# Optimization experiments

Measured on AMD Instinct MI355X. Metric: run time of the kernel, lower is better.

Reference implementation:

```python
import jax, jax.numpy as jnp
import numpy as np

H = 1024          # hidden_size
A = 8             # num_actions
T = 64            # timesteps
N = 256           # batch (num envs)


def _gru_cell(x, h, Wih, Whh, bih, bhh):
    # torch.nn.GRUCell math; gate order (r, z, n)
    gi = x @ Wih.T + bih           # [N, 3H]
    gh = h @ Whh.T + bhh           # [N, 3H]
    i_r, i_z, i_n = jnp.split(gi, 3, axis=1)
    h_r, h_z, h_n = jnp.split(gh, 3, axis=1)
    r = jax.nn.sigmoid(i_r + h_r)
    z = jax.nn.sigmoid(i_z + h_z)
    n = jnp.tanh(i_n + r * h_n)
    return (1.0 - z) * n + z * h


def setup_inputs() -> dict:
    key = jax.random.key(0)
    ks = jax.random.split(key, 12)
    s = 0.02
    return {
        "c": jax.random.normal(ks[0], (T * N, H), jnp.float32),
        "hxs": jax.random.normal(ks[1], (N, 3 * H), jnp.float32),
        "masks": jnp.ones((T * N, 1), jnp.float32),
        "prev_action_one_hot": jnp.zeros((T * N, A), jnp.float32).at[jnp.arange(T * N), jax.random.randint(ks[2], (T * N,), 0, A)].set(1.0),
        "h_gru_Wih": s * jax.random.normal(ks[3], (3 * H, H), jnp.float32),
        "h_gru_Whh": s * jax.random.normal(ks[4], (3 * H, H), jnp.float32),
        "h_gru_bih": jnp.zeros((3 * H,), jnp.float32),
        "h_gru_bhh": jnp.zeros((3 * H,), jnp.float32),
        "f_gru_Wih": s * jax.random.normal(ks[5], (3 * H, H), jnp.float32),
        "f_gru_Whh": s * jax.random.normal(ks[6], (3 * H, H), jnp.float32),
        "f_gru_bih": jnp.zeros((3 * H,), jnp.float32),
        "f_gru_bhh": jnp.zeros((3 * H,), jnp.float32),
        "p_W": s * jax.random.normal(ks[7], (2 * H, 2 * H + A), jnp.float32),
        "p_b": jnp.zeros((2 * H,), jnp.float32),
        "q_W": s * jax.random.normal(ks[8], (2 * H, 2 * H + A), jnp.float32),
        "q_b": jnp.zeros((2 * H,), jnp.float32),
    }


def reference(c, hxs, masks, prev_action_one_hot,
              h_gru_Wih, h_gru_Whh, h_gru_bih, h_gru_bhh,
              f_gru_Wih, f_gru_Whh, f_gru_bih, f_gru_bhh,
              p_W, p_b, q_W, q_b):
    c3 = c.reshape(T, N, H)
    m3 = masks.reshape(T, N, 1)
    a3 = prev_action_one_hot.reshape(T, N, A)
    f0 = hxs[:, :H]
    h0 = hxs[:, H:2 * H]
    q0 = hxs[:, 2 * H:]

    def step(carry, xs):
        f, h, q_mu = carry
        c_t, m_t, a_t = xs
        p_in = jnp.concatenate([h, q_mu, a_t], axis=1) * m_t
        p_dist = p_in @ p_W.T + p_b                     # [N, 2H]
        p_mu = p_dist[:, :H]
        q_in = jnp.concatenate([f, c_t, a_t], axis=1) * m_t
        q_dist = q_in @ q_W.T + q_b                     # [N, 2H]
        q_mu_new = q_dist[:, :H]
        f_new = _gru_cell(c_t, f * m_t, f_gru_Wih, f_gru_Whh, f_gru_bih, f_gru_bhh)
        h_new = _gru_cell(p_mu, h * m_t, h_gru_Wih, h_gru_Whh, h_gru_bih, h_gru_bhh)
        return (f_new, h_new, q_mu_new), (p_dist, q_dist)

    (f, h, q_mu), (p_all, q_all) = jax.lax.scan(step, (f0, h0, q0), (c3, m3, a3))
    acc_p = p_all.reshape(T * N, 2 * H)
    acc_q = q_all.reshape(T * N, 2 * H)
    hxs_out = jnp.concatenate([f, h, q_mu], axis=1)
    return acc_p, acc_q, hxs_out
```

## Files before the change

kernel.cpp:

```cpp
#include <hip/hip_runtime.h>
#include <math.h>

typedef __attribute__((ext_vector_type(8))) __bf16 bf16x8;
typedef __attribute__((ext_vector_type(4))) float f32x4;

constexpr int H = 1024, T = 64, NB = 256, TWOH = 2048, THREEH = 3072;
constexpr long long OFF_Q  = 33554432LL;
constexpr long long OFF_HX = 67108864LL;
constexpr int LA = 6;

constexpr int R_PWH = 0, R_PWQ = 2048, R_QWF = 4096, R_QWC = 6144,
              R_FWIH = 8192, R_FWHH = 11264, R_HWIH = 14336, R_HWHH = 17408;

#define LD4(p) (*reinterpret_cast<const float4*>(p))

__device__ __forceinline__ float sigf(float x) { return 1.0f / (1.0f + expf(-x)); }

__device__ __forceinline__ void gload16(const void* g, void* l) {
    __builtin_amdgcn_global_load_lds(
        (const __attribute__((address_space(1))) uint32_t*)g,
        (__attribute__((address_space(3))) uint32_t*)l, 16, 0, 0);
}

__device__ __forceinline__ void st_bf_swz(__bf16* base, int n, int k, float v) {
    base[(size_t)n * 1024 + (((k >> 3) ^ (n & 7)) << 3) + (k & 7)] = (__bf16)v;
}

__device__ __forceinline__ void swz_rc(int i, int NR, int& rt, int& ct) {
    const int k = i & 7;
    const int m = i >> 3;
    ct = k + 8 * (m / NR);
    rt = m % NR;
}

#define FRAGOFF(rloc, gl) (((rloc) << 7) + ((((gl)) ^ ((rloc) & 7)) << 4))

template<int RT>
__device__ __forceinline__ void stage_tile(const char* g, char* l, int kb, int tid) {
    #pragma unroll
    for (int i = 0; i < RT / 32; ++i) {
        const int L = i * 4096 + tid * 16;
        gload16(g + (size_t)(L >> 7) * 2048 + (size_t)kb * 128 + (L & 127), l + L);
    }
}

__device__ __forceinline__ void mm128(
    int tid, char* sA, char* sB,
    const char* A, const char* B,
    f32x4 (&acc)[2][4])
{
    const int lane = tid & 63, w = tid >> 6;
    const int l15 = lane & 15, lg = lane >> 4;
    const int wr = w >> 1, wc = w & 1;
    int aoff[2][2], boff[4][2];
    #pragma unroll
    for (int fr = 0; fr < 2; ++fr)
        #pragma unroll
        for (int kk = 0; kk < 2; ++kk)
            aoff[fr][kk] = FRAGOFF(wr * 32 + fr * 16 + l15, kk * 4 + lg);
    #pragma unroll
    for (int fc = 0; fc < 4; ++fc)
        #pragma unroll
        for (int kk = 0; kk < 2; ++kk)
            boff[fc][kk] = FRAGOFF(wc * 64 + fc * 16 + l15, kk * 4 + lg);

    stage_tile<64>(A, sA, 0, tid);
    stage_tile<128>(B, sB, 0, tid);
    stage_tile<64>(A, sA + 8192, 1, tid);
    stage_tile<128>(B, sB + 16384, 1, tid);
    for (int kb = 0; kb < 16; ++kb) {
        const int kn = kb + 2;
        if (kn < 16) {
            const int bo = kn % 3;
            stage_tile<64>(A, sA + bo * 8192, kn, tid);
            stage_tile<128>(B, sB + bo * 16384, kn, tid);
            asm volatile("s_waitcnt vmcnt(12)" ::: "memory");
        } else if (kb + 1 < 16) {
            asm volatile("s_waitcnt vmcnt(6)" ::: "memory");
        } else {
            asm volatile("s_waitcnt vmcnt(0)" ::: "memory");
        }
        __builtin_amdgcn_s_barrier();
        __builtin_amdgcn_sched_barrier(0);
        const int bc = kb % 3;
        char* Ab = sA + bc * 8192;
        char* Bb = sB + bc * 16384;
        bf16x8 af[2][2], bv[4][2];
        #pragma unroll
        for (int fr = 0; fr < 2; ++fr)
            #pragma unroll
            for (int kk = 0; kk < 2; ++kk)
                af[fr][kk] = *reinterpret_cast<const bf16x8*>(Ab + aoff[fr][kk]);
        #pragma unroll
        for (int fc = 0; fc < 4; ++fc)
            #pragma unroll
            for (int kk = 0; kk < 2; ++kk)
                bv[fc][kk] = *reinterpret_cast<const bf16x8*>(Bb + boff[fc][kk]);
        __builtin_amdgcn_s_setprio(1);
        #pragma unroll
        for (int kk = 0; kk < 2; ++kk)
            #pragma unroll
            for (int fr = 0; fr < 2; ++fr)
                #pragma unroll
                for (int fc = 0; fc < 4; ++fc)
                    acc[fr][fc] = __builtin_amdgcn_mfma_f32_16x16x32_bf16(
                        af[fr][kk], bv[fc][kk], acc[fr][fc], 0, 0, 0);
        __builtin_amdgcn_s_setprio(0);
        __builtin_amdgcn_s_barrier();
        __builtin_amdgcn_sched_barrier(0);
    }
}

__device__ __forceinline__ void mm32g1(
    int tid, char* sA, char* sB,
    const char* A, const char* Bg,
    f32x4 (&aR)[2], f32x4 (&aZ)[2], f32x4 (&aN)[2])
{
    const int lane = tid & 63, w = tid >> 6;
    const int l15 = lane & 15, lg = lane >> 4;
    const int wr = w >> 1, wc = w & 1;
    int aoff[2], boff[2][2];
    #pragma unroll
    for (int kk = 0; kk < 2; ++kk)
        aoff[kk] = FRAGOFF(wr * 16 + l15, kk * 4 + lg);
    #pragma unroll
    for (int fc = 0; fc < 2; ++fc)
        #pragma unroll
        for (int kk = 0; kk < 2; ++kk)
            boff[fc][kk] = FRAGOFF(wc * 32 + fc * 16 + l15, kk * 4 + lg);

    auto stg = [&](int buf, int kb) {
        stage_tile<32>(A, sA + buf * 4096, kb, tid);
        #pragma unroll
        for (int g = 0; g < 3; ++g)
            stage_tile<64>(Bg + (size_t)g * 2097152, sB + buf * 24576 + g * 8192, kb, tid);
    };
    stg(0, 0);
    for (int kb = 0; kb < 16; ++kb) {
        if (kb + 1 < 16) {
            stg((kb + 1) & 1, kb + 1);
            asm volatile("s_waitcnt vmcnt(7)" ::: "memory");
        } else {
            asm volatile("s_waitcnt vmcnt(0)" ::: "memory");
        }
        __builtin_amdgcn_s_barrier();
        __builtin_amdgcn_sched_barrier(0);
        char* Ab = sA + (kb & 1) * 4096;
        char* Bb = sB + (kb & 1) * 24576;
        bf16x8 af[2];
        #pragma unroll
        for (int kk = 0; kk < 2; ++kk)
            af[kk] = *reinterpret_cast<const bf16x8*>(Ab + aoff[kk]);
        bf16x8 bvr[2][2], bvz[2][2], bvn[2][2];
        #pragma unroll
        for (int fc = 0; fc < 2; ++fc)
            #pragma unroll
            for (int kk = 0; kk < 2; ++kk) {
                bvr[fc][kk] = *reinterpret_cast<const bf16x8*>(Bb + boff[fc][kk]);
                bvz[fc][kk] = *reinterpret_cast<const bf16x8*>(Bb + 8192 + boff[fc][kk]);
                bvn[fc][kk] = *reinterpret_cast<const bf16x8*>(Bb + 16384 + boff[fc][kk]);
            }
        __builtin_amdgcn_s_setprio(1);
        #pragma unroll
        for (int kk = 0; kk < 2; ++kk)
            #pragma unroll
            for (int fc = 0; fc < 2; ++fc) {
                aR[fc] = __builtin_amdgcn_mfma_f32_16x16x32_bf16(af[kk], bvr[fc][kk], aR[fc], 0, 0, 0);
                aZ[fc] = __builtin_amdgcn_mfma_f32_16x16x32_bf16(af[kk], bvz[fc][kk], aZ[fc], 0, 0, 0);
                aN[fc] = __builtin_amdgcn_mfma_f32_16x16x32_bf16(af[kk], bvn[fc][kk], aN[fc], 0, 0, 0);
            }
        __builtin_amdgcn_s_setprio(0);
        __builtin_amdgcn_s_barrier();
        __builtin_amdgcn_sched_barrier(0);
    }
}

__device__ __forceinline__ void do_xq(int slice, int i, int tid, char* sA, char* sB,
    const char* cbfB, const char* Wb, const float* act, const float* qW, float* out)
{
    const int lane = tid & 63, w = tid >> 6;
    const int l15 = lane & 15, lg = lane >> 4;
    const int wr = w >> 1, wc = w & 1;
    int rt, ct; swz_rc(i, 4, rt, ct);
    const int row0 = rt * 64, col0 = ct * 128;
    const size_t grow0 = (size_t)slice * NB + row0;
    f32x4 acc[2][4] = {};
    mm128(tid, sA, sB, cbfB + grow0 * 2048, Wb + (size_t)(R_QWC + col0) * 2048, acc);
    #pragma unroll
    for (int fc = 0; fc < 4; ++fc) {
        const int gc = col0 + wc * 64 + fc * 16 + l15;
        const float* wp = qW + (size_t)gc * 2056 + 2048;
        float4 x0 = LD4(wp), x1 = LD4(wp + 4);
        #pragma unroll
        for (int fr = 0; fr < 2; ++fr)
            #pragma unroll
            for (int j = 0; j < 4; ++j) {
                const size_t n = grow0 + wr * 32 + fr * 16 + lg * 4 + j;
                const float* ar = act + n * 8;
                float4 a0 = LD4(ar), a1 = LD4(ar + 4);
                float dot = a0.x * x0.x + a0.y * x0.y + a0.z * x0.z + a0.w * x0.w
                          + a1.x * x1.x + a1.y * x1.y + a1.z * x1.z + a1.w * x1.w;
                out[OFF_Q + n * TWOH + gc] = acc[fr][fc][j] + dot;
            }
    }
}

__device__ __forceinline__ void do_gf(int slice, int i, int tid, char* sA, char* sB,
    const char* cbfB, const char* Wb, __bf16* Gfb)
{
    const int lane = tid & 63, w = tid >> 6;
    const int l15 = lane & 15, lg = lane >> 4;
    const int wr = w >> 1, wc = w & 1;
    int rt, ct; swz_rc(i, 4, rt, ct);
    const int row0 = rt * 64, col0 = ct * 128;
    f32x4 acc[2][4] = {};
    mm128(tid, sA, sB, cbfB + ((size_t)slice * NB + row0) * 2048,
          Wb + (size_t)(R_FWIH + col0) * 2048, acc);
    __bf16* gdst = Gfb + (size_t)(slice & 7) * NB * THREEH;
    #pragma unroll
    for (int fc = 0; fc < 4; ++fc) {
        const int gc = col0 + wc * 64 + fc * 16 + l15;
        #pragma unroll
        for (int fr = 0; fr < 2; ++fr)
            #pragma unroll
            for (int j = 0; j < 4; ++j) {
                const int n = row0 + wr * 32 + fr * 16 + lg * 4 + j;
                gdst[(size_t)n * THREEH + gc] = (__bf16)acc[fr][fc][j];
            }
    }
}

__device__ __forceinline__ void do_pq(int tt, int i, int tid, char* sA, char* sB,
    const __bf16* qmu_t, const char* Wb, const float* masks, const float* act,
    const float* pW, const float* pb, float* out)
{
    const int lane = tid & 63, w = tid >> 6;
    const int l15 = lane & 15, lg = lane >> 4;
    const int wr = w >> 1, wc = w & 1;
    int rt, ct; swz_rc(i, 4, rt, ct);
    const int row0 = rt * 64, col0 = ct * 128;
    f32x4 acc[2][4] = {};
    mm128(tid, sA, sB, (const char*)qmu_t + (size_t)row0 * 2048,
          Wb + (size_t)(R_PWQ + col0) * 2048, acc);
    const float* mrow = masks + (size_t)tt * NB;
    float* ob = out + (size_t)tt * NB * TWOH;
    #pragma unroll
    for (int fc = 0; fc < 4; ++fc) {
        const int gc = col0 + wc * 64 + fc * 16 + l15;
        const float* wp = pW + (size_t)gc * 2056 + 2048;
        float4 x0 = LD4(wp), x1 = LD4(wp + 4);
        const float bb = pb[gc];
        #pragma unroll
        for (int fr = 0; fr < 2; ++fr)
            #pragma unroll
            for (int j = 0; j < 4; ++j) {
                const int n = row0 + wr * 32 + fr * 16 + lg * 4 + j;
                const float* ar = act + ((size_t)tt * NB + n) * 8;
                float4 a0 = LD4(ar), a1 = LD4(ar + 4);
                float dot = a0.x * x0.x + a0.y * x0.y + a0.z * x0.z + a0.w * x0.w
                          + a1.x * x1.x + a1.y * x1.y + a1.z * x1.z + a1.w * x1.w;
                ob[(size_t)n * TWOH + gc] = acc[fr][fc][j] + mrow[n] * dot + bb;
            }
    }
}

__global__ __launch_bounds__(256) void wcvt_k(
    const float* __restrict__ pW, const float* __restrict__ qW,
    const float* __restrict__ fWih, const float* __restrict__ fWhh,
    const float* __restrict__ hWih, const float* __restrict__ hWhh,
    __bf16* __restrict__ Wbf)
{
    const long i = (long)blockIdx.x * 256 + threadIdx.x;
    const int row = (int)(i >> 7);
    const int G   = (int)i & 127;
    const float* src; int stride; int koff = 0; int r;
    if (row < 2048)       { src = pW;   stride = 2056; koff = 0;    r = row; }
    else if (row < 4096)  { src = pW;   stride = 2056; koff = 1024; r = row - 2048; }
    else if (row < 6144)  { src = qW;   stride = 2056; koff = 0;    r = row - 4096; }
    else if (row < 8192)  { src = qW;   stride = 2056; koff = 1024; r = row - 6144; }
    else if (row < 11264) { src = fWih; stride = 1024; r = row - 8192; }
    else if (row < 14336) { src = fWhh; stride = 1024; r = row - 11264; }
    else if (row < 17408) { src = hWih; stride = 1024; r = row - 14336; }
    else                  { src = hWhh; stride = 1024; r = row - 17408; }
    const float* p = src + (long)r * stride + koff + G * 8;
    float4 a = LD4(p), b = LD4(p + 4);
    bf16x8 v;
    v[0] = (__bf16)a.x; v[1] = (__bf16)a.y; v[2] = (__bf16)a.z; v[3] = (__bf16)a.w;
    v[4] = (__bf16)b.x; v[5] = (__bf16)b.y; v[6] = (__bf16)b.z; v[7] = (__bf16)b.w;
    *reinterpret_cast<bf16x8*>(Wbf + (size_t)row * 1024 + ((G ^ (row & 7)) << 3)) = v;
}

__global__ __launch_bounds__(256) void ccvt_k(const float* __restrict__ c,
                                              __bf16* __restrict__ cbf) {
    const long i = (long)blockIdx.x * 256 + threadIdx.x;
    const int row = (int)(i >> 7);
    const int G   = (int)i & 127;
    const float* p = c + (size_t)row * 1024 + G * 8;
    float4 a = LD4(p), b = LD4(p + 4);
    bf16x8 v;
    v[0] = (__bf16)a.x; v[1] = (__bf16)a.y; v[2] = (__bf16)a.z; v[3] = (__bf16)a.w;
    v[4] = (__bf16)b.x; v[5] = (__bf16)b.y; v[6] = (__bf16)b.z; v[7] = (__bf16)b.w;
    *reinterpret_cast<bf16x8*>(cbf + (size_t)row * 1024 + ((G ^ (row & 7)) << 3)) = v;
}

__global__ __launch_bounds__(256) void init2_k(
    const float* __restrict__ hxs, const float* __restrict__ masks,
    float* __restrict__ fst0, float* __restrict__ hst0,
    __bf16* __restrict__ fbm0, __bf16* __restrict__ hbm0, __bf16* __restrict__ qmub0)
{
    const int idx = blockIdx.x * 256 + threadIdx.x;
    const int arr = idx >> 15;
    const int g   = idx & 32767;
    const int n   = g >> 7;
    const int G   = g & 127;
    const float m0 = masks[n];
    const float* p = hxs + (size_t)n * THREEH + arr * 1024 + G * 8;
    float4 a = LD4(p), b = LD4(p + 4);
    __bf16* dstB = arr == 0 ? fbm0 : (arr == 1 ? hbm0 : qmub0);
    bf16x8 v;
    v[0] = (__bf16)(a.x * m0); v[1] = (__bf16)(a.y * m0);
    v[2] = (__bf16)(a.z * m0); v[3] = (__bf16)(a.w * m0);
    v[4] = (__bf16)(b.x * m0); v[5] = (__bf16)(b.y * m0);
    v[6] = (__bf16)(b.z * m0); v[7] = (__bf16)(b.w * m0);
    *reinterpret_cast<bf16x8*>(dstB + (size_t)n * 1024 + ((G ^ (n & 7)) << 3)) = v;
    if (arr < 2) {
        float* dstF = arr == 0 ? fst0 : hst0;
        *reinterpret_cast<float4*>(dstF + (size_t)n * 1024 + G * 8) = a;
        *reinterpret_cast<float4*>(dstF + (size_t)n * 1024 + G * 8 + 4) = b;
    }
}

__global__ __launch_bounds__(256) void pre_k(
    const char* __restrict__ cbfB, const char* __restrict__ Wb,
    const float* __restrict__ act, const float* __restrict__ qW,
    const __bf16* __restrict__ qmb0, const float* __restrict__ masks,
    const float* __restrict__ pW, const float* __restrict__ pb,
    __bf16* __restrict__ Gfb, float* __restrict__ out)
{
    __shared__ char smem[73728];
    if (blockIdx.x < LA * 160) {
        const int s = blockIdx.x / 160;
        const int i = blockIdx.x % 160;
        if (i < 64) do_xq(s, i, threadIdx.x, smem, smem + 24576, cbfB, Wb, act, qW, out);
        else        do_gf(s, i - 64, threadIdx.x, smem, smem + 24576, cbfB, Wb, Gfb);
    } else {
        do_pq(0, blockIdx.x - LA * 160, threadIdx.x, smem, smem + 24576,
              qmb0, Wb, masks, act, pW, pb, out);
    }
}

__global__ __launch_bounds__(256) void k1_k(
    int t,
    const __bf16* __restrict__ hbm, const __bf16* __restrict__ fbm,
    __bf16* __restrict__ qmubN,
    const float* __restrict__ masks, const float* __restrict__ act,
    const float* __restrict__ qb, const float* __restrict__ qW,
    const char* __restrict__ Wb,
    __bf16* __restrict__ pmub, float* __restrict__ Shh,
    const __bf16* __restrict__ Gfb,
    const float* __restrict__ fbih, const float* __restrict__ fbhh,
    const float* __restrict__ fstF, float* __restrict__ fstN, __bf16* __restrict__ fbmN,
    float* __restrict__ out)
{
    __shared__ char smem[73728];
    char* sA = smem;
    char* sB = smem + 24576;
    const int tid = threadIdx.x;
    const int lane = tid & 63, w = tid >> 6;
    const int l15 = lane & 15, lg = lane >> 4;
    const int wr = w >> 1, wc = w & 1;
    const float* mrow = masks + (size_t)t * NB;
    const float* mn   = masks + (size_t)(t + 1 < T ? t + 1 : t) * NB;
    int b = blockIdx.x;

    if (b < 64) {
        int rt, ct; swz_rc(b, 4, rt, ct);
        const int row0 = rt * 64, col0 = ct * 128;
        f32x4 acc[2][4] = {};
        mm128(tid, sA, sB, (const char*)hbm + (size_t)row0 * 2048,
              Wb + (size_t)(R_PWH + col0) * 2048, acc);
        float* ob = out + (size_t)t * NB * TWOH;
        #pragma unroll
        for (int fc = 0; fc < 4; ++fc) {
            const int gc = col0 + wc * 64 + fc * 16 + l15;
            #pragma unroll
            for (int fr = 0; fr < 2; ++fr)
                #pragma unroll
                for (int j = 0; j < 4; ++j) {
                    const int n = row0 + wr * 32 + fr * 16 + lg * 4 + j;
                    const float v = ob[(size_t)n * TWOH + gc] + acc[fr][fc][j];
                    ob[(size_t)n * TWOH + gc] = v;
                    if (gc < 1024) st_bf_swz(pmub, n, gc, v);
                }
        }
    } else if (b < 128) {
        int rt, ct; swz_rc(b - 64, 4, rt, ct);
        const int row0 = rt * 64, col0 = ct * 128;
        f32x4 acc[2][4] = {};
        mm128(tid, sA, sB, (const char*)fbm + (size_t)row0 * 2048,
              Wb + (size_t)(R_QWF + col0) * 2048, acc);
        float* ob = out + OFF_Q + (size_t)t * NB * TWOH;
        #pragma unroll
        for (int fc = 0; fc < 4; ++fc) {
            const int gc = col0 + wc * 64 + fc * 16 + l15;
            const float bb = qb[gc];
            #pragma unroll
            for (int fr = 0; fr < 2; ++fr)
                #pragma unroll
                for (int j = 0; j < 4; ++j) {
                    const int n = row0 + wr * 32 + fr * 16 + lg * 4 + j;
                    const float xq = ob[(size_t)n * TWOH + gc];
                    float v = acc[fr][fc][j] + mrow[n] * xq + bb;
                    ob[(size_t)n * TWOH + gc] = v;
                    if (gc < 1024) st_bf_swz(qmubN, n, gc, v * mn[n]);
                }
        }
    } else if (b < 224) {
        int rt, ct; swz_rc(b - 128, 4, rt, ct);
        const int row0 = rt * 64, col0 = ct * 128;
        f32x4 acc[2][4] = {};
        mm128(tid, sA, sB, (const char*)hbm + (size_t)row0 * 2048,
              Wb + (size_t)(R_HWHH + col0) * 2048, acc);
        #pragma unroll
        for (int fc = 0; fc < 4; ++fc) {
            const int gc = col0 + wc * 64 + fc * 16 + l15;
            #pragma unroll
            for (int fr = 0; fr < 2; ++fr)
                #pragma unroll
                for (int j = 0; j < 4; ++j) {
                    const int n = row0 + wr * 32 + fr * 16 + lg * 4 + j;
                    Shh[(size_t)n * THREEH + gc] = acc[fr][fc][j];
                }
        }
    } else {
        int rt, ct; swz_rc(b - 224, 8, rt, ct);
        const int row0 = rt * 32, col0 = ct * 64;
        f32x4 aR[2] = {}, aZ[2] = {}, aN[2] = {};
        mm32g1(tid, sA, sB, (const char*)fbm + (size_t)row0 * 2048,
               Wb + (size_t)(R_FWHH + col0) * 2048, aR, aZ, aN);
        const __bf16* gsl = Gfb + (size_t)(t & 7) * NB * THREEH;
        #pragma unroll
        for (int fc = 0; fc < 2; ++fc) {
            const int col = col0 + wc * 32 + fc * 16 + l15;
            const float br  = fbih[col] + fbhh[col];
            const float bz  = fbih[col + 1024] + fbhh[col + 1024];
            const float bni = fbih[col + 2048], bnh = fbhh[col + 2048];
            #pragma unroll
            for (int j = 0; j < 4; ++j) {
                const int n = row0 + wr * 16 + lg * 4 + j;
                const float gfr = (float)gsl[(size_t)n * THREEH + col];
                const float gfz = (float)gsl[(size_t)n * THREEH + col + 1024];
                const float gfn = (float)gsl[(size_t)n * THREEH + col + 2048];
                const float rg = sigf(gfr + aR[fc][j] + br);
                const float zg = sigf(gfz + aZ[fc][j] + bz);
                const float ng = tanhf(gfn + bni + rg * (aN[fc][j] + bnh));
                const float fm = fstF[(size_t)n * 1024 + col] * mrow[n];
                const float o = (1.f - zg) * ng + zg * fm;
                fstN[(size_t)n * 1024 + col] = o;
                st_bf_swz(fbmN, n, col, o * mn[n]);
            }
        }
    }
}

__global__ __launch_bounds__(256) void k2_k(
    int t,
    const __bf16* __restrict__ pmub, const __bf16* __restrict__ qmubN,
    const char* __restrict__ cbfB,
    const float* __restrict__ Shh,
    const float* __restrict__ hstF, float* __restrict__ hstN, __bf16* __restrict__ hbmN,
    const char* __restrict__ Wb,
    const float* __restrict__ hbih, const float* __restrict__ hbhh,
    const float* __restrict__ masks, const float* __restrict__ act,
    const float* __restrict__ pW, const float* __restrict__ pb,
    const float* __restrict__ qW,
    __bf16* __restrict__ Gfb, float* __restrict__ out)
{
    __shared__ char smem[73728];
    char* sA = smem;
    char* sB = smem + 24576;
    const int tid = threadIdx.x;
    const int lane = tid & 63, w = tid >> 6;
    const int l15 = lane & 15, lg = lane >> 4;
    const int wr = w >> 1, wc = w & 1;
    const float* mrow = masks + (size_t)t * NB;
    const float* mn   = masks + (size_t)(t + 1 < T ? t + 1 : t) * NB;
    const int b = blockIdx.x;

    if (b < 128) {
        int rt, ct; swz_rc(b, 8, rt, ct);
        const int row0 = rt * 32, col0 = ct * 64;
        f32x4 aR[2] = {}, aZ[2] = {}, aN[2] = {};
        mm32g1(tid, sA, sB, (const char*)pmub + (size_t)row0 * 2048,
               Wb + (size_t)(R_HWIH + col0) * 2048, aR, aZ, aN);
        #pragma unroll
        for (int fc = 0; fc < 2; ++fc) {
            const int col = col0 + wc * 32 + fc * 16 + l15;
            const float bri = hbih[col],        brh = hbhh[col];
            const float bzi = hbih[col + 1024], bzh = hbhh[col + 1024];
            const float bni = hbih[col + 2048], bnh = hbhh[col + 2048];
            #pragma unroll
            for (int j = 0; j < 4; ++j) {
                const int n = row0 + wr * 16 + lg * 4 + j;
                const float ghr = Shh[(size_t)n * THREEH + col];
                const float ghz = Shh[(size_t)n * THREEH + col + 1024];
                const float ghn = Shh[(size_t)n * THREEH + col + 2048];
                const float rg = sigf(aR[fc][j] + bri + ghr + brh);
                const float zg = sigf(aZ[fc][j] + bzi + ghz + bzh);
                const float ng = tanhf(aN[fc][j] + bni + rg * (ghn + bnh));
                const float hm = hstF[(size_t)n * 1024 + col] * mrow[n];
                const float o = (1.f - zg) * ng + zg * hm;
                hstN[(size_t)n * 1024 + col] = o;
                st_bf_swz(hbmN, n, col, o * mn[n]);
            }
        }
    } else if (b < 192) {
        if (t + 1 < T)
            do_pq(t + 1, b - 128, tid, sA, sB, qmubN, Wb, masks, act, pW, pb, out);
    } else if (b < 256) {
        if (t + LA < T)
            do_xq(t + LA, b - 192, tid, sA, sB, cbfB, Wb, act, qW, out);
    } else {
        if (t + LA < T)
            do_gf(t + LA, b - 256, tid, sA, sB, cbfB, Wb, Gfb);
    }
}

__global__ __launch_bounds__(256) void write_hxs_k(const float* __restrict__ fS,
                                                   const float* __restrict__ hS,
                                                   float* out) {
    const int i = blockIdx.x * 256 + threadIdx.x;
    const int n = i / THREEH;
    const int j = i - n * THREEH;
    float v;
    if (j < H)          v = fS[(size_t)n * H + j];
    else if (j < TWOH)  v = hS[(size_t)n * H + (j - H)];
    else                v = out[OFF_Q + ((size_t)(T - 1) * NB + n) * TWOH + (j - TWOH)];
    out[OFF_HX + i] = v;
}

extern "C" void kernel_launch(void* const* d_in, const int* in_sizes, int n_in,
                              void* d_out, int out_size, void* d_ws, size_t ws_size,
                              hipStream_t stream) {
    (void)in_sizes; (void)n_in; (void)out_size; (void)ws_size;

    const float* c     = (const float*)d_in[0];
    const float* hxs   = (const float*)d_in[1];
    const float* masks = (const float*)d_in[2];
    const float* act   = (const float*)d_in[3];
    const float* hWih  = (const float*)d_in[4];
    const float* hWhh  = (const float*)d_in[5];
    const float* hbih  = (const float*)d_in[6];
    const float* hbhh  = (const float*)d_in[7];
    const float* fWih  = (const float*)d_in[8];
    const float* fWhh  = (const float*)d_in[9];
    const float* fbih  = (const float*)d_in[10];
    const float* fbhh  = (const float*)d_in[11];
    const float* pW    = (const float*)d_in[12];
    const float* pb    = (const float*)d_in[13];
    const float* qW    = (const float*)d_in[14];
    const float* qb    = (const float*)d_in[15];

    float* out = (float*)d_out;
    char*  wsb = (char*)d_ws;

    __bf16* Wbf  = (__bf16*)(wsb);
    __bf16* cbf  = (__bf16*)(wsb + 41943040LL);
    float*  fst[2] = { (float*)(wsb + 75497472LL), (float*)(wsb + 76546048LL) };
    float*  hst[2] = { (float*)(wsb + 77594624LL), (float*)(wsb + 78643200LL) };
    __bf16* fbm[2] = { (__bf16*)(wsb + 79691776LL), (__bf16*)(wsb + 80216064LL) };
    __bf16* hbm[2] = { (__bf16*)(wsb + 80740352LL), (__bf16*)(wsb + 81264640LL) };
    __bf16* qmb[2] = { (__bf16*)(wsb + 81788928LL), (__bf16*)(wsb + 82313216LL) };
    __bf16* pmub   = (__bf16*)(wsb + 82837504LL);
    float*  Shh    = (float*)(wsb + 83361792LL);
    __bf16* Gfb    = (__bf16*)(wsb + 86507520LL);
    const char* Wb   = (const char*)Wbf;
    const char* cbfB = (const char*)cbf;

    wcvt_k <<<dim3(10240), dim3(256), 0, stream>>>(pW, qW, fWih, fWhh, hWih, hWhh, Wbf);
    ccvt_k <<<dim3(8192),  dim3(256), 0, stream>>>(c, cbf);
    init2_k<<<dim3(384),   dim3(256), 0, stream>>>(hxs, masks, fst[0], hst[0],
                                                   fbm[0], hbm[0], qmb[0]);
    pre_k  <<<dim3(LA * 160 + 64), dim3(256), 0, stream>>>(
        cbfB, Wb, act, qW, qmb[0], masks, pW, pb, Gfb, out);

    for (int t = 0; t < T; ++t) {
        const int cur = t & 1, nxt = cur ^ 1;
        k1_k<<<dim3(352), dim3(256), 0, stream>>>(
            t, hbm[cur], fbm[cur], qmb[nxt],
            masks, act, qb, qW, Wb, pmub, Shh, Gfb,
            fbih, fbhh, fst[cur], fst[nxt], fbm[nxt], out);
        k2_k<<<dim3(352), dim3(256), 0, stream>>>(
            t, pmub, qmb[nxt], cbfB, Shh,
            hst[cur], hst[nxt], hbm[nxt],
            Wb, hbih, hbhh, masks, act, pW, pb, qW, Gfb, out);
    }

    write_hxs_k<<<dim3(3072), dim3(256), 0, stream>>>(fst[0], hst[0], out);
}
```

Baseline: 2.144 ms.

## Hoist all xq GEMMs to pre-kernel, use 64-row fused-gate GRU tiles, rebalance k1/k2

The c-only q projection (xq) for all 64 timesteps now runs in one large pre-kernel instead of being interleaved per step. The GRU gate GEMMs switch from 32x64 tiles to 64-row tiles whose r/z/n weight rows are interleaved in the weight conversion, so one contiguous B tile feeds all three gates and the block count drops. The f-GRU update moves from k1 to k2, and gf lookahead work is split across both kernels, shrinking each per-step launch to 256 blocks. Tile-index swizzling is replaced with plain row-major mapping. This trades the L2-friendly swizzle and some parallelism for less per-step work and better reuse of operands.

After: 2.506 ms. 1.17x slower.

```diff
diff --git a/kernel.cpp b/kernel.cpp
--- a/kernel.cpp
+++ b/kernel.cpp
@@ -24,13 +24,6 @@
 
 __device__ __forceinline__ void st_bf_swz(__bf16* base, int n, int k, float v) {
     base[(size_t)n * 1024 + (((k >> 3) ^ (n & 7)) << 3) + (k & 7)] = (__bf16)v;
-}
-
-__device__ __forceinline__ void swz_rc(int i, int NR, int& rt, int& ct) {
-    const int k = i & 7;
-    const int m = i >> 3;
-    ct = k + 8 * (m / NR);
-    rt = m % NR;
 }
 
 #define FRAGOFF(rloc, gl) (((rloc) << 7) + ((((gl)) ^ ((rloc) & 7)) << 4))
@@ -111,64 +104,73 @@
     }
 }
 
-__device__ __forceinline__ void mm32g1(
+__device__ __forceinline__ void mm64g(
     int tid, char* sA, char* sB,
-    const char* A, const char* Bg,
-    f32x4 (&aR)[2], f32x4 (&aZ)[2], f32x4 (&aN)[2])
+    const char* A, const char* Bp,
+    f32x4 (&aR)[2][2], f32x4 (&aZ)[2][2], f32x4 (&aN)[2][2])
 {
     const int lane = tid & 63, w = tid >> 6;
     const int l15 = lane & 15, lg = lane >> 4;
     const int wr = w >> 1, wc = w & 1;
-    int aoff[2], boff[2][2];
-    #pragma unroll
-    for (int kk = 0; kk < 2; ++kk)
-        aoff[kk] = FRAGOFF(wr * 16 + l15, kk * 4 + lg);
-    #pragma unroll
-    for (int fc = 0; fc < 2; ++fc)
+    int aoff[2][2], boff[2][3][2];
+    #pragma unroll
+    for (int fr = 0; fr < 2; ++fr)
         #pragma unroll
         for (int kk = 0; kk < 2; ++kk)
-            boff[fc][kk] = FRAGOFF(wc * 32 + fc * 16 + l15, kk * 4 + lg);
-
+            aoff[fr][kk] = FRAGOFF(wr * 32 + fr * 16 + l15, kk * 4 + lg);
+    #pragma unroll
+    for (int cb = 0; cb < 2; ++cb)
+        #pragma unroll
+        for (int g = 0; g < 3; ++g)
+            #pragma unroll
+            for (int kk = 0; kk < 2; ++kk) {
+                const int v = wc * 96 + (cb * 3 + g) * 16 + l15;
+                boff[cb][g][kk] = FRAGOFF(v, kk * 4 + lg);
+            }
     auto stg = [&](int buf, int kb) {
-        stage_tile<32>(A, sA + buf * 4096, kb, tid);
-        #pragma unroll
-        for (int g = 0; g < 3; ++g)
-            stage_tile<64>(Bg + (size_t)g * 2097152, sB + buf * 24576 + g * 8192, kb, tid);
+        stage_tile<64>(A, sA + buf * 8192, kb, tid);
+        stage_tile<192>(Bp, sB + buf * 24576, kb, tid);
     };
     stg(0, 0);
     for (int kb = 0; kb < 16; ++kb) {
         if (kb + 1 < 16) {
             stg((kb + 1) & 1, kb + 1);
-            asm volatile("s_waitcnt vmcnt(7)" ::: "memory");
+            asm volatile("s_waitcnt vmcnt(8)" ::: "memory");
         } else {
             asm volatile("s_waitcnt vmcnt(0)" ::: "memory");
         }
         __builtin_amdgcn_s_barrier();
         __builtin_amdgcn_sched_barrier(0);
-        char* Ab = sA + (kb & 1) * 4096;
+        char* Ab = sA + (kb & 1) * 8192;
         char* Bb = sB + (kb & 1) * 24576;
-        bf16x8 af[2];
+        bf16x8 af[2][2];
+        #pragma unroll
+        for (int fr = 0; fr < 2; ++fr)
+            #pragma unroll
+            for (int kk = 0; kk < 2; ++kk)
+                af[fr][kk] = *reinterpret_cast<const bf16x8*>(Ab + aoff[fr][kk]);
+        bf16x8 bv[2][3][2];
+        #pragma unroll
+        for (int cb = 0; cb < 2; ++cb)
+            #pragma unroll
+            for (int g = 0; g < 3; ++g)
+                #pragma unroll
+                for (int kk = 0; kk < 2; ++kk)
+                    bv[cb][g][kk] = *reinterpret_cast<const bf16x8*>(Bb + boff[cb][g][kk]);
+        __builtin_amdgcn_s_setprio(1);
         #pragma unroll
         for (int kk = 0; kk < 2; ++kk)
-            af[kk] = *reinterpret_cast<const bf16x8*>(Ab + aoff[kk]);
-        bf16x8 bvr[2][2], bvz[2][2], bvn[2][2];
-        #pragma unroll
-        for (int fc = 0; fc < 2; ++fc)
-            #pragma unroll
-            for (int kk = 0; kk < 2; ++kk) {
-                bvr[fc][kk] = *reinterpret_cast<const bf16x8*>(Bb + boff[fc][kk]);
-                bvz[fc][kk] = *reinterpret_cast<const bf16x8*>(Bb + 8192 + boff[fc][kk]);
-                bvn[fc][kk] = *reinterpret_cast<const bf16x8*>(Bb + 16384 + boff[fc][kk]);
-            }
-        __builtin_amdgcn_s_setprio(1);
-        #pragma unroll
-        for (int kk = 0; kk < 2; ++kk)
-            #pragma unroll
-            for (int fc = 0; fc < 2; ++fc) {
-                aR[fc] = __builtin_amdgcn_mfma_f32_16x16x32_bf16(af[kk], bvr[fc][kk], aR[fc], 0, 0, 0);
-                aZ[fc] = __builtin_amdgcn_mfma_f32_16x16x32_bf16(af[kk], bvz[fc][kk], aZ[fc], 0, 0, 0);
-                aN[fc] = __builtin_amdgcn_mfma_f32_16x16x32_bf16(af[kk], bvn[fc][kk], aN[fc], 0, 0, 0);
-            }
+            #pragma unroll
+            for (int fr = 0; fr < 2; ++fr)
+                #pragma unroll
+                for (int cb = 0; cb < 2; ++cb) {
+                    aR[fr][cb] = __builtin_amdgcn_mfma_f32_16x16x32_bf16(
+                        af[fr][kk], bv[cb][0][kk], aR[fr][cb], 0, 0, 0);
+                    aZ[fr][cb] = __builtin_amdgcn_mfma_f32_16x16x32_bf16(
+                        af[fr][kk], bv[cb][1][kk], aZ[fr][cb], 0, 0, 0);
+                    aN[fr][cb] = __builtin_amdgcn_mfma_f32_16x16x32_bf16(
+                        af[fr][kk], bv[cb][2][kk], aN[fr][cb], 0, 0, 0);
+                }
         __builtin_amdgcn_s_setprio(0);
         __builtin_amdgcn_s_barrier();
         __builtin_amdgcn_sched_barrier(0);
@@ -181,8 +183,7 @@
     const int lane = tid & 63, w = tid >> 6;
     const int l15 = lane & 15, lg = lane >> 4;
     const int wr = w >> 1, wc = w & 1;
-    int rt, ct; swz_rc(i, 4, rt, ct);
-    const int row0 = rt * 64, col0 = ct * 128;
+    const int row0 = (i >> 4) * 64, col0 = (i & 15) * 128;
     const size_t grow0 = (size_t)slice * NB + row0;
     f32x4 acc[2][4] = {};
     mm128(tid, sA, sB, cbfB + grow0 * 2048, Wb + (size_t)(R_QWC + col0) * 2048, acc);
@@ -211,8 +212,7 @@
     const int lane = tid & 63, w = tid >> 6;
     const int l15 = lane & 15, lg = lane >> 4;
     const int wr = w >> 1, wc = w & 1;
-    int rt, ct; swz_rc(i, 4, rt, ct);
-    const int row0 = rt * 64, col0 = ct * 128;
+    const int row0 = (i / 24) * 64, col0 = (i % 24) * 128;
     f32x4 acc[2][4] = {};
     mm128(tid, sA, sB, cbfB + ((size_t)slice * NB + row0) * 2048,
           Wb + (size_t)(R_FWIH + col0) * 2048, acc);
@@ -237,8 +237,7 @@
     const int lane = tid & 63, w = tid >> 6;
     const int l15 = lane & 15, lg = lane >> 4;
     const int wr = w >> 1, wc = w & 1;
-    int rt, ct; swz_rc(i, 4, rt, ct);
-    const int row0 = rt * 64, col0 = ct * 128;
+    const int row0 = (i >> 4) * 64, col0 = (i & 15) * 128;
     f32x4 acc[2][4] = {};
     mm128(tid, sA, sB, (const char*)qmu_t + (size_t)row0 * 2048,
           Wb + (size_t)(R_PWQ + col0) * 2048, acc);
@@ -279,8 +278,20 @@
     else if (row < 6144)  { src = qW;   stride = 2056; koff = 0;    r = row - 4096; }
     else if (row < 8192)  { src = qW;   stride = 2056; koff = 1024; r = row - 6144; }
     else if (row < 11264) { src = fWih; stride = 1024; r = row - 8192; }
-    else if (row < 14336) { src = fWhh; stride = 1024; r = row - 11264; }
-    else if (row < 17408) { src = hWih; stride = 1024; r = row - 14336; }
+    else if (row < 14336) {
+        const int rp = row - 11264;
+        const int j = rp / 192, rem = rp % 192;
+        const int chunk = rem / 48, rem2 = rem % 48;
+        const int g = rem2 >> 4, cc = rem2 & 15;
+        src = fWhh; stride = 1024; r = g * 1024 + j * 64 + chunk * 16 + cc;
+    }
+    else if (row < 17408) {
+        const int rp = row - 14336;
+        const int j = rp / 192, rem = rp % 192;
+        const int chunk = rem / 48, rem2 = rem % 48;
+        const int g = rem2 >> 4, cc = rem2 & 15;
+        src = hWih; stride = 1024; r = g * 1024 + j * 64 + chunk * 16 + cc;
+    }
     else                  { src = hWhh; stride = 1024; r = row - 17408; }
     const float* p = src + (long)r * stride + koff + G * 8;
     float4 a = LD4(p), b = LD4(p + 4);
@@ -338,13 +349,14 @@
     __bf16* __restrict__ Gfb, float* __restrict__ out)
 {
     __shared__ char smem[73728];
-    if (blockIdx.x < LA * 160) {
-        const int s = blockIdx.x / 160;
-        const int i = blockIdx.x % 160;
-        if (i < 64) do_xq(s, i, threadIdx.x, smem, smem + 24576, cbfB, Wb, act, qW, out);
-        else        do_gf(s, i - 64, threadIdx.x, smem, smem + 24576, cbfB, Wb, Gfb);
+    const int b = blockIdx.x;
+    if (b < 4096) {
+        do_xq(b >> 6, b & 63, threadIdx.x, smem, smem + 24576, cbfB, Wb, act, qW, out);
+    } else if (b < 4096 + LA * 96) {
+        const int r = b - 4096;
+        do_gf(r / 96, r % 96, threadIdx.x, smem, smem + 24576, cbfB, Wb, Gfb);
     } else {
-        do_pq(0, blockIdx.x - LA * 160, threadIdx.x, smem, smem + 24576,
+        do_pq(0, b - 4096 - LA * 96, threadIdx.x, smem, smem + 24576,
               qmb0, Wb, masks, act, pW, pb, out);
     }
 }
@@ -352,14 +364,12 @@
 __global__ __launch_bounds__(256) void k1_k(
     int t,
     const __bf16* __restrict__ hbm, const __bf16* __restrict__ fbm,
-    __bf16* __restrict__ qmubN,
+    __bf16* __restrict__ qmubN, const char* __restrict__ cbfB,
     const float* __restrict__ masks, const float* __restrict__ act,
     const float* __restrict__ qb, const float* __restrict__ qW,
     const char* __restrict__ Wb,
     __bf16* __restrict__ pmub, float* __restrict__ Shh,
-    const __bf16* __restrict__ Gfb,
-    const float* __restrict__ fbih, const float* __restrict__ fbhh,
-    const float* __restrict__ fstF, float* __restrict__ fstN, __bf16* __restrict__ fbmN,
+    __bf16* __restrict__ Gfb,
     float* __restrict__ out)
 {
     __shared__ char smem[73728];
@@ -374,8 +384,7 @@
     int b = blockIdx.x;
 
     if (b < 64) {
-        int rt, ct; swz_rc(b, 4, rt, ct);
-        const int row0 = rt * 64, col0 = ct * 128;
+        const int row0 = (b >> 4) * 64, col0 = (b & 15) * 128;
         f32x4 acc[2][4] = {};
         mm128(tid, sA, sB, (const char*)hbm + (size_t)row0 * 2048,
               Wb + (size_t)(R_PWH + col0) * 2048, acc);
@@ -394,8 +403,8 @@
                 }
         }
     } else if (b < 128) {
-        int rt, ct; swz_rc(b - 64, 4, rt, ct);
-        const int row0 = rt * 64, col0 = ct * 128;
+        b -= 64;
+        const int row0 = (b >> 4) * 64, col0 = (b & 15) * 128;
         f32x4 acc[2][4] = {};
         mm128(tid, sA, sB, (const char*)fbm + (size_t)row0 * 2048,
               Wb + (size_t)(R_QWF + col0) * 2048, acc);
@@ -416,8 +425,8 @@
                 }
         }
     } else if (b < 224) {
-        int rt, ct; swz_rc(b - 128, 4, rt, ct);
-        const int row0 = rt * 64, col0 = ct * 128;
+        const int i = b - 128;
+        const int row0 = (i / 24) * 64, col0 = (i % 24) * 128;
         f32x4 acc[2][4] = {};
         mm128(tid, sA, sB, (const char*)hbm + (size_t)row0 * 2048,
               Wb + (size_t)(R_HWHH + col0) * 2048, acc);
@@ -433,44 +442,21 @@
                 }
         }
     } else {
-        int rt, ct; swz_rc(b - 224, 8, rt, ct);
-        const int row0 = rt * 32, col0 = ct * 64;
-        f32x4 aR[2] = {}, aZ[2] = {}, aN[2] = {};
-        mm32g1(tid, sA, sB, (const char*)fbm + (size_t)row0 * 2048,
-               Wb + (size_t)(R_FWHH + col0) * 2048, aR, aZ, aN);
-        const __bf16* gsl = Gfb + (size_t)(t & 7) * NB * THREEH;
-        #pragma unroll
-        for (int fc = 0; fc < 2; ++fc) {
-            const int col = col0 + wc * 32 + fc * 16 + l15;
-            const float br  = fbih[col] + fbhh[col];
-            const float bz  = fbih[col + 1024] + fbhh[col + 1024];
-            const float bni = fbih[col + 2048], bnh = fbhh[col + 2048];
-            #pragma unroll
-            for (int j = 0; j < 4; ++j) {
-                const int n = row0 + wr * 16 + lg * 4 + j;
-                const float gfr = (float)gsl[(size_t)n * THREEH + col];
-                const float gfz = (float)gsl[(size_t)n * THREEH + col + 1024];
-                const float gfn = (float)gsl[(size_t)n * THREEH + col + 2048];
-                const float rg = sigf(gfr + aR[fc][j] + br);
-                const float zg = sigf(gfz + aZ[fc][j] + bz);
-                const float ng = tanhf(gfn + bni + rg * (aN[fc][j] + bnh));
-                const float fm = fstF[(size_t)n * 1024 + col] * mrow[n];
-                const float o = (1.f - zg) * ng + zg * fm;
-                fstN[(size_t)n * 1024 + col] = o;
-                st_bf_swz(fbmN, n, col, o * mn[n]);
-            }
-        }
+        if (t + LA < T)
+            do_gf(t + LA, b - 224, tid, sA, sB, cbfB, Wb, Gfb);
     }
 }
 
 __global__ __launch_bounds__(256) void k2_k(
     int t,
     const __bf16* __restrict__ pmub, const __bf16* __restrict__ qmubN,
-    const char* __restrict__ cbfB,
+    const __bf16* __restrict__ fbm, const char* __restrict__ cbfB,
     const float* __restrict__ Shh,
     const float* __restrict__ hstF, float* __restrict__ hstN, __bf16* __restrict__ hbmN,
+    const float* __restrict__ fstF, float* __restrict__ fstN, __bf16* __restrict__ fbmN,
     const char* __restrict__ Wb,
     const float* __restrict__ hbih, const float* __restrict__ hbhh,
+    const float* __restrict__ fbih, const float* __restrict__ fbhh,
     const float* __restrict__ masks, const float* __restrict__ act,
     const float* __restrict__ pW, const float* __restrict__ pb,
     const float* __restrict__ qW,
@@ -487,42 +473,70 @@
     const float* mn   = masks + (size_t)(t + 1 < T ? t + 1 : t) * NB;
     const int b = blockIdx.x;
 
-    if (b < 128) {
-        int rt, ct; swz_rc(b, 8, rt, ct);
-        const int row0 = rt * 32, col0 = ct * 64;
-        f32x4 aR[2] = {}, aZ[2] = {}, aN[2] = {};
-        mm32g1(tid, sA, sB, (const char*)pmub + (size_t)row0 * 2048,
-               Wb + (size_t)(R_HWIH + col0) * 2048, aR, aZ, aN);
-        #pragma unroll
-        for (int fc = 0; fc < 2; ++fc) {
-            const int col = col0 + wc * 32 + fc * 16 + l15;
+    if (b < 64) {
+        const int row0 = (b >> 4) * 64, col0 = (b & 15) * 64;
+        f32x4 aR[2][2] = {}, aZ[2][2] = {}, aN[2][2] = {};
+        mm64g(tid, sA, sB, (const char*)pmub + (size_t)row0 * 2048,
+              Wb + (size_t)(R_HWIH + (b & 15) * 192) * 2048, aR, aZ, aN);
+        #pragma unroll
+        for (int cb = 0; cb < 2; ++cb) {
+            const int col = col0 + wc * 32 + cb * 16 + l15;
             const float bri = hbih[col],        brh = hbhh[col];
             const float bzi = hbih[col + 1024], bzh = hbhh[col + 1024];
             const float bni = hbih[col + 2048], bnh = hbhh[col + 2048];
             #pragma unroll
-            for (int j = 0; j < 4; ++j) {
-                const int n = row0 + wr * 16 + lg * 4 + j;
-                const float ghr = Shh[(size_t)n * THREEH + col];
-                const float ghz = Shh[(size_t)n * THREEH + col + 1024];
-                const float ghn = Shh[(size_t)n * THREEH + col + 2048];
-                const float rg = sigf(aR[fc][j] + bri + ghr + brh);
-                const float zg = sigf(aZ[fc][j] + bzi + ghz + bzh);
-                const float ng = tanhf(aN[fc][j] + bni + rg * (ghn + bnh));
-                const float hm = hstF[(size_t)n * 1024 + col] * mrow[n];
-                const float o = (1.f - zg) * ng + zg * hm;
-                hstN[(size_t)n * 1024 + col] = o;
-                st_bf_swz(hbmN, n, col, o * mn[n]);
-            }
+            for (int fr = 0; fr < 2; ++fr)
+                #pragma unroll
+                for (int j = 0; j < 4; ++j) {
+                    const int n = row0 + wr * 32 + fr * 16 + lg * 4 + j;
+                    const float ghr = Shh[(size_t)n * THREEH + col];
+                    const float ghz = Shh[(size_t)n * THREEH + col + 1024];
+                    const float ghn = Shh[(size_t)n * THREEH + col + 2048];
+                    const float rg = sigf(aR[fr][cb][j] + bri + ghr + brh);
+                    const float zg = sigf(aZ[fr][cb][j] + bzi + ghz + bzh);
+                    const float ng = tanhf(aN[fr][cb][j] + bni + rg * (ghn + bnh));
+                    const float hm = hstF[(size_t)n * 1024 + col] * mrow[n];
+                    const float o = (1.f - zg) * ng + zg * hm;
+                    hstN[(size_t)n * 1024 + col] = o;
+                    st_bf_swz(hbmN, n, col, o * mn[n]);
+                }
+        }
+    } else if (b < 128) {
+        const int i = b - 64;
+        const int row0 = (i >> 4) * 64, col0 = (i & 15) * 64;
+        f32x4 aR[2][2] = {}, aZ[2][2] = {}, aN[2][2] = {};
+        mm64g(tid, sA, sB, (const char*)fbm + (size_t)row0 * 2048,
+              Wb + (size_t)(R_FWHH + (i & 15) * 192) * 2048, aR, aZ, aN);
+        const __bf16* gsl = Gfb + (size_t)(t & 7) * NB * THREEH;
+        #pragma unroll
+        for (int cb = 0; cb < 2; ++cb) {
+            const int col = col0 + wc * 32 + cb * 16 + l15;
+            const float br  = fbih[col] + fbhh[col];
+            const float bz  = fbih[col + 1024] + fbhh[col + 1024];
+            const float bni = fbih[col + 2048], bnh = fbhh[col + 2048];
+            #pragma unroll
+            for (int fr = 0; fr < 2; ++fr)
+                #pragma unroll
+                for (int j = 0; j < 4; ++j) {
+                    const int n = row0 + wr * 32 + fr * 16 + lg * 4 + j;
+                    const float gfr = (float)gsl[(size_t)n * THREEH + col];
+                    const float gfz = (float)gsl[(size_t)n * THREEH + col + 1024];
+                    const float gfn = (float)gsl[(size_t)n * THREEH + col + 2048];
+                    const float rg = sigf(gfr + aR[fr][cb][j] + br);
+                    const float zg = sigf(gfz + aZ[fr][cb][j] + bz);
+                    const float ng = tanhf(gfn + bni + rg * (aN[fr][cb][j] + bnh));
+                    const float fm = fstF[(size_t)n * 1024 + col] * mrow[n];
+                    const float o = (1.f - zg) * ng + zg * fm;
+                    fstN[(size_t)n * 1024 + col] = o;
+                    st_bf_swz(fbmN, n, col, o * mn[n]);
+                }
         }
     } else if (b < 192) {
         if (t + 1 < T)
             do_pq(t + 1, b - 128, tid, sA, sB, qmubN, Wb, masks, act, pW, pb, out);
-    } else if (b < 256) {
-        if (t + LA < T)
-            do_xq(t + LA, b - 192, tid, sA, sB, cbfB, Wb, act, qW, out);
     } else {
         if (t + LA < T)
-            do_gf(t + LA, b - 256, tid, sA, sB, cbfB, Wb, Gfb);
+            do_gf(t + LA, (b - 192) + 32, tid, sA, sB, cbfB, Wb, Gfb);
     }
 }
 
@@ -581,19 +595,19 @@
     ccvt_k <<<dim3(8192),  dim3(256), 0, stream>>>(c, cbf);
     init2_k<<<dim3(384),   dim3(256), 0, stream>>>(hxs, masks, fst[0], hst[0],
                                                    fbm[0], hbm[0], qmb[0]);
-    pre_k  <<<dim3(LA * 160 + 64), dim3(256), 0, stream>>>(
+    pre_k  <<<dim3(4096 + LA * 96 + 64), dim3(256), 0, stream>>>(
         cbfB, Wb, act, qW, qmb[0], masks, pW, pb, Gfb, out);
 
     for (int t = 0; t < T; ++t) {
         const int cur = t & 1, nxt = cur ^ 1;
-        k1_k<<<dim3(352), dim3(256), 0, stream>>>(
-            t, hbm[cur], fbm[cur], qmb[nxt],
-            masks, act, qb, qW, Wb, pmub, Shh, Gfb,
-            fbih, fbhh, fst[cur], fst[nxt], fbm[nxt], out);
-        k2_k<<<dim3(352), dim3(256), 0, stream>>>(
-            t, pmub, qmb[nxt], cbfB, Shh,
+        k1_k<<<dim3(256), dim3(256), 0, stream>>>(
+            t, hbm[cur], fbm[cur], qmb[nxt], cbfB,
+            masks, act, qb, qW, Wb, pmub, Shh, Gfb, out);
+        k2_k<<<dim3(256), dim3(256), 0, stream>>>(
+            t, pmub, qmb[nxt], fbm[cur], cbfB, Shh,
             hst[cur], hst[nxt], hbm[nxt],
-            Wb, hbih, hbhh, masks, act, pW, pb, qW, Gfb, out);
+            fst[cur], fst[nxt], fbm[nxt],
+            Wb, hbih, hbhh, fbih, fbhh, masks, act, pW, pb, qW, Gfb, out);
     }
 
     write_hxs_k<<<dim3(3072), dim3(256), 0, stream>>>(fst[0], hst[0], out);
```
